# Optimization experiments

Measured on AMD Instinct MI355X. Metric: run time of the kernel, lower is better.

## Reference

```python
import jax, jax.numpy as jnp
import numpy as np

H = 51  # n_hidden
B = 8192  # batch
T = 2048  # seq_len
FUTURE = 64


def setup_inputs() -> dict:
    key = jax.random.key(0)
    ks = jax.random.split(key, 12)
    s = 1.0 / np.sqrt(H)
    u = lambda k, shape: jax.random.uniform(k, shape, jnp.float32, -s, s)
    return {
        "x": jax.random.normal(ks[0], (B, T), jnp.float32),
        "W_ih1": u(ks[1], (4 * H, 1)),
        "W_hh1": u(ks[2], (4 * H, H)),
        "b_ih1": u(ks[3], (4 * H,)),
        "b_hh1": u(ks[4], (4 * H,)),
        "W_ih2": u(ks[5], (4 * H, H)),
        "W_hh2": u(ks[6], (4 * H, H)),
        "b_ih2": u(ks[7], (4 * H,)),
        "b_hh2": u(ks[8], (4 * H,)),
        "W_out": u(ks[9], (1, H)),
        "b_out": u(ks[10], (1,)),
        "future": FUTURE,
    }


def _lstm_cell(x, h, c, Wih, Whh, bih, bhh):
    # PyTorch LSTMCell: gates ordered i, f, g, o
    g = x @ Wih.T + h @ Whh.T + (bih + bhh)  # [B, 4H]
    i, f, gg, o = jnp.split(g, 4, axis=-1)
    i = jax.nn.sigmoid(i)
    f = jax.nn.sigmoid(f)
    gg = jnp.tanh(gg)
    o = jax.nn.sigmoid(o)
    c2 = f * c + i * gg
    h2 = o * jnp.tanh(c2)
    return h2, c2


def reference(x, W_ih1, W_hh1, b_ih1, b_hh1, W_ih2, W_hh2, b_ih2, b_hh2,
              W_out, b_out, future):
    Bn = x.shape[0]
    h1 = jnp.zeros((Bn, H), x.dtype)
    c1 = jnp.zeros((Bn, H), x.dtype)

    def emit(h1, c1):
        # Quirk of the original code: layer-2 state is layer-1's CURRENT (h1, c1),
        # and layer-2's own state is never carried forward.
        h2, _ = _lstm_cell(h1, h1, c1, W_ih2, W_hh2, b_ih2, b_hh2)
        return h2 @ W_out.T + b_out  # [B, 1]

    def step(carry, xt):
        h1, c1 = carry
        h1, c1 = _lstm_cell(xt, h1, c1, W_ih1, W_hh1, b_ih1, b_hh1)
        out = emit(h1, c1)
        return (h1, c1), out

    xs = jnp.swapaxes(x, 0, 1)[:, :, None]  # [T, B, 1]
    (h1, c1), outs = jax.lax.scan(step, (h1, c1), xs)
    outs = outs[..., 0].T  # [B, T]

    def fstep(carry, _):
        h1, c1, out = carry
        h1, c1 = _lstm_cell(out, h1, c1, W_ih1, W_hh1, b_ih1, b_hh1)
        out = emit(h1, c1)
        return (h1, c1, out), out

    last = outs[:, -1:]
    _, fouts = jax.lax.scan(fstep, (h1, c1, last), None, length=future)
    fouts = fouts[..., 0].T if future > 0 else jnp.zeros((Bn, 0), x.dtype)
    return jnp.concatenate([outs, fouts], axis=1)  # [B, T + future]
```

## Files before the change

### kernel.cpp

```cpp
#include <hip/hip_runtime.h>

#define HH   51
#define H4   204
#define TSEQ 2048
#define FUT  64
#define TT   (TSEQ + FUT)
#define RPB  16
#define NTH  1024
#define HSTR 72

typedef _Float16 h8 __attribute__((ext_vector_type(8)));
typedef float    f4 __attribute__((ext_vector_type(4)));

#define LOG2E 1.44269504f
#define MFMA(a, b, c) __builtin_amdgcn_mfma_f32_16x16x32_f16(a, b, c, 0, 0, 0)

__device__ __forceinline__ void act_cell(const f4 g, float cin, float* cout, float* hout) {
    const float ei = __builtin_amdgcn_exp2f(g[0]);
    const float ef = __builtin_amdgcn_exp2f(g[1]);
    const float eg = __builtin_amdgcn_exp2f(g[2]);
    const float eo = __builtin_amdgcn_exp2f(g[3]);
    const float A = 1.0f + ei, B = 1.0f + ef, G = 1.0f + eg, C = 1.0f + eo;
    const float rAB = __builtin_amdgcn_rcpf(A * B);
    const float ig = rAB * B;
    const float fg = rAB * A;
    const float rGC = __builtin_amdgcn_rcpf(G * C);
    const float og = rGC * G;
    const float tg = __builtin_fmaf(2.0f, rGC * C, -1.0f);
    const float c2 = __builtin_fmaf(fg, cin, ig * tg);
    const float ec = __builtin_amdgcn_exp2f(-2.0f * LOG2E * c2);
    const float th = __builtin_fmaf(2.0f, __builtin_amdgcn_rcpf(1.0f + ec), -1.0f);
    *cout = c2;
    *hout = og * th;
}

#define MERGED_BODY(P, EMIT_IDX, DO_EMIT, XI)                                      \
    do {                                                                           \
        if (is_comp) {                                                             \
            const h8 b0 = *(const h8*)&hbuf[P][nl][quad * 8];                      \
            const h8 b1 = *(const h8*)&hbuf[P][nl][32 + quad * 8];                 \
            f4 G1 = {0.f, 0.f, 0.f, 0.f}, G2 = {0.f, 0.f, 0.f, 0.f};               \
            G2 = MFMA(W2[0], b0, G2); G2 = MFMA(W2[1], b1, G2);                    \
            G1 = MFMA(W1[0], b0, G1); G1 = MFMA(W1[1], b1, G1);                    \
            float c2v, h2v;                                                        \
            act_cell(G2, c1, &c2v, &h2v);         \
            part[(P) ^ 1][cw][quad][nl] = h2v * wo;                                \
            float hv;                                                              \
            act_cell(G1, c1, &c1, &hv);                     \
            if (kh < HH) hbuf[(P) ^ 1][nl][1 + kh] = (_Float16)hv;                 \
        } else if (w == we) {                                                      \
            if ((DO_EMIT) && lane < RPB) {                                         \
                float s0 = bo, s1 = 0.f, s2 = 0.f, s3 = 0.f;                       \
                _Pragma("unroll")                                                  \
                for (int j = 0; j < 13; ++j) {                                     \
                    s0 += part[P][j][0][lane];                                     \
                    s1 += part[P][j][1][lane];                                     \
                    s2 += part[P][j][2][lane];                                     \
                    s3 += part[P][j][3][lane];                                     \
                }                                                                  \
                out[(size_t)(rb + lane) * TT + (EMIT_IDX)] = (s0 + s1) + (s2 + s3);\
            }                                                                      \
        } else if (w == wp && lane < RPB) {                                        \
            if ((XI) + 1 < TSEQ) hbuf[(P) ^ 1][lane][0] = (_Float16)xnext;         \
            if ((XI) + 2 < TSEQ) xnext = x[(size_t)(rb + lane) * TSEQ + (XI) + 2]; \
        }                                                                          \
        __syncthreads();                                                           \
    } while (0)

__global__ __launch_bounds__(NTH, 8)
void lstm_kernel(const float* __restrict__ x,
                 const float* __restrict__ Wih1, const float* __restrict__ Whh1,
                 const float* __restrict__ bih1, const float* __restrict__ bhh1,
                 const float* __restrict__ Wih2, const float* __restrict__ Whh2,
                 const float* __restrict__ bih2, const float* __restrict__ bhh2,
                 const float* __restrict__ Wout, const float* __restrict__ bout,
                 float* __restrict__ out)
{
    __shared__ _Float16 hbuf[2][RPB][HSTR];
    __shared__ float part[2][13][4][17];
    __shared__ float wouts[64];

    const int tid  = threadIdx.x;
    const int lane = tid & 63;
    const int w    = tid >> 6;
    const int quad = lane >> 4;
    const int nl   = lane & 15;
    const int rb   = blockIdx.x * RPB;

    const int  rot     = (blockIdx.x >> 8) & 1;
    const int  cw      = w - (rot ? 3 : 0);
    const bool is_comp = (cw >= 0) && (cw < 13);
    const int  we      = rot ? 0 : 13;
    const int  wp      = rot ? 1 : 14;

    if (tid < 64) wouts[tid] = (tid < HH) ? Wout[tid] : 0.0f;
    for (int i = tid; i < 2 * RPB * HSTR; i += NTH) (&hbuf[0][0][0])[i] = (_Float16)0.0f;
    __syncthreads();
    if (tid < RPB) {
        hbuf[0][tid][0]  = (_Float16)x[(size_t)(rb + tid) * TSEQ];
        hbuf[0][tid][52] = (_Float16)1.0f;  hbuf[0][tid][53] = (_Float16)1.0f;
        hbuf[1][tid][52] = (_Float16)1.0f;  hbuf[1][tid][53] = (_Float16)1.0f;
    }
    const float bo = bout[0];

    h8 W1[2], W2[2];
    if (is_comp) {
        const int jp = 16 * cw + nl;
        const int kk = jp >> 2, q = jp & 3;
        const bool valid = (jp < H4);
        const int jrow = q * HH + kk;
        const float sc = (q == 2) ? (-2.0f * LOG2E) : (-LOG2E);
        float b1 = 0.0f, b2 = 0.0f;
        if (valid) { b1 = sc * (bih1[jrow] + bhh1[jrow]); b2 = sc * (bih2[jrow] + bhh2[jrow]); }
        const _Float16 b1h = (_Float16)b1, b2h = (_Float16)b2;
        const _Float16 b1l = (_Float16)(b1 - (float)b1h), b2l = (_Float16)(b2 - (float)b2h);
        #pragma unroll
        for (int s = 0; s < 2; ++s) {
            h8 w1v, w2v;
            #pragma unroll
            for (int j = 0; j < 8; ++j) {
                const int k = s * 32 + quad * 8 + j;
                _Float16 a1 = (_Float16)0.0f, a2 = (_Float16)0.0f;
                if (valid) {
                    if (k == 0) {
                        a1 = (_Float16)(sc * Wih1[jrow]);
                    } else if (k <= HH) {
                        const int o = jrow * HH + (k - 1);
                        a1 = (_Float16)(sc * Whh1[o]);
                        a2 = (_Float16)(sc * (Wih2[o] + Whh2[o]));
                    } else if (k == 52) { a1 = b1h; a2 = b2h; }
                    else if (k == 53)   { a1 = b1l; a2 = b2l; }
                }
                w1v[j] = a1;
                w2v[j] = a2;
            }
            W1[s] = w1v;
            W2[s] = w2v;
        }
    }

    float xnext = 0.0f;
    if (w == wp && lane < RPB) xnext = x[(size_t)(rb + lane) * TSEQ + 1];

    const int kh = 4 * cw + quad;
    float c1 = 0.0f;
    __syncthreads();
    const float wo = is_comp ? wouts[kh] : 0.0f;

    if (is_comp) {
        const h8 b0 = *(const h8*)&hbuf[0][nl][quad * 8];
        const h8 b1 = *(const h8*)&hbuf[0][nl][32 + quad * 8];
        f4 G1 = {0.f, 0.f, 0.f, 0.f};
        G1 = MFMA(W1[0], b0, G1); G1 = MFMA(W1[1], b1, G1);
        float hv;
        act_cell(G1, c1, &c1, &hv);
        if (kh < HH) hbuf[1][nl][1 + kh] = (_Float16)hv;
    } else if (w == wp && lane < RPB) {
        hbuf[1][lane][0] = (_Float16)xnext;
        xnext = x[(size_t)(rb + lane) * TSEQ + 2];
    }
    __syncthreads();

    MERGED_BODY(1, 0, false, 1);

    for (int i = 2; i < TSEQ; i += 2) {
        MERGED_BODY(0, i - 2, true, i);
        MERGED_BODY(1, i - 1, true, i + 1);
    }

    for (int t = TSEQ - 1; t < TT; ++t) {
        const int pb = (t + 1) & 1;
        if (is_comp) {
            const h8 b0 = *(const h8*)&hbuf[pb][nl][quad * 8];
            const h8 b1 = *(const h8*)&hbuf[pb][nl][32 + quad * 8];
            f4 G2 = {0.f, 0.f, 0.f, 0.f};
            G2 = MFMA(W2[0], b0, G2); G2 = MFMA(W2[1], b1, G2);
            float c2v, h2v;
            act_cell(G2, c1, &c2v, &h2v);
            part[t & 1][cw][quad][nl] = h2v * wo;
        } else if (w == we && t == TSEQ - 1 && lane < RPB) {
            float s0 = bo, s1 = 0.f, s2 = 0.f, s3 = 0.f;
            #pragma unroll
            for (int j = 0; j < 13; ++j) {
                s0 += part[0][j][0][lane];
                s1 += part[0][j][1][lane];
                s2 += part[0][j][2][lane];
                s3 += part[0][j][3][lane];
            }
            out[(size_t)(rb + lane) * TT + (TSEQ - 2)] = (s0 + s1) + (s2 + s3);
        }
        __syncthreads();
        if (w == we && lane < RPB) {
            float s0 = bo, s1 = 0.f, s2 = 0.f, s3 = 0.f;
            #pragma unroll
            for (int j = 0; j < 13; ++j) {
                s0 += part[t & 1][j][0][lane];
                s1 += part[t & 1][j][1][lane];
                s2 += part[t & 1][j][2][lane];
                s3 += part[t & 1][j][3][lane];
            }
            const float s = (s0 + s1) + (s2 + s3);
            out[(size_t)(rb + lane) * TT + t] = s;
            if (t + 1 < TT) hbuf[pb][lane][0] = (_Float16)s;
        }
        __syncthreads();
        if (t + 1 < TT) {
            if (is_comp) {
                const h8 b0 = *(const h8*)&hbuf[pb][nl][quad * 8];
                const h8 b1 = *(const h8*)&hbuf[pb][nl][32 + quad * 8];
                f4 G1 = {0.f, 0.f, 0.f, 0.f};
                G1 = MFMA(W1[0], b0, G1); G1 = MFMA(W1[1], b1, G1);
                float hv;
                act_cell(G1, c1, &c1, &hv);
                if (kh < HH) hbuf[pb ^ 1][nl][1 + kh] = (_Float16)hv;
            }
            __syncthreads();
        }
    }
}

extern "C" void kernel_launch(void* const* d_in, const int* in_sizes, int n_in,
                              void* d_out, int out_size, void* d_ws, size_t ws_size,
                              hipStream_t stream) {
    (void)in_sizes; (void)n_in; (void)d_ws; (void)ws_size; (void)out_size;
    const float* x    = (const float*)d_in[0];
    const float* Wih1 = (const float*)d_in[1];
    const float* Whh1 = (const float*)d_in[2];
    const float* bih1 = (const float*)d_in[3];
    const float* bhh1 = (const float*)d_in[4];
    const float* Wih2 = (const float*)d_in[5];
    const float* Whh2 = (const float*)d_in[6];
    const float* bih2 = (const float*)d_in[7];
    const float* bhh2 = (const float*)d_in[8];
    const float* Wout = (const float*)d_in[9];
    const float* bout = (const float*)d_in[10];
    float* outp = (float*)d_out;

    dim3 grid(8192 / RPB);
    dim3 block(NTH);
    hipLaunchKernelGGL(lstm_kernel, grid, block, 0, stream,
                       x, Wih1, Whh1, bih1, bhh1, Wih2, Whh2, bih2, bhh2,
                       Wout, bout, outp);
}
```

Baseline: 2.502 ms.

## Defer layer-2 emit activation by one step and merge aux warps

```diff
diff --git a/kernel.cpp b/kernel.cpp
--- a/kernel.cpp
+++ b/kernel.cpp
@@ -6,7 +6,7 @@
 #define FUT  64
 #define TT   (TSEQ + FUT)
 #define RPB  16
-#define NTH  1024
+#define NTH  896
 #define HSTR 72
 
 typedef _Float16 h8 __attribute__((ext_vector_type(8)));
@@ -34,35 +34,54 @@
     *hout = og * th;
 }
 
-#define MERGED_BODY(P, EMIT_IDX, DO_EMIT, XI)                                      \
+__device__ __forceinline__ void act_emit(const f4 g, float cin, float* hout) {
+    const float ei = __builtin_amdgcn_exp2f(g[0]);
+    const float ef = __builtin_amdgcn_exp2f(g[1]);
+    const float eg = __builtin_amdgcn_exp2f(g[2]);
+    const float eo = __builtin_amdgcn_exp2f(g[3]);
+    const float A = 1.0f + ei, B = 1.0f + ef, G = 1.0f + eg, C = 1.0f + eo;
+    const float P1 = A * B, P2 = G * C;
+    const float r = __builtin_amdgcn_rcpf(P1 * P2);
+    const float rP2 = r * P2, rP1 = r * P1;
+    const float ig = rP2 * B;
+    const float fg = rP2 * A;
+    const float og = rP1 * G;
+    const float tg = __builtin_fmaf(2.0f, rP1 * C, -1.0f);
+    const float c2 = __builtin_fmaf(fg, cin, ig * tg);
+    const float ec = __builtin_amdgcn_exp2f(-2.0f * LOG2E * c2);
+    const float th = __builtin_fmaf(2.0f, __builtin_amdgcn_rcpf(1.0f + ec), -1.0f);
+    *hout = og * th;
+}
+
+#define MBODY(P, i)                                                                \
     do {                                                                           \
         if (is_comp) {                                                             \
             const h8 b0 = *(const h8*)&hbuf[P][nl][quad * 8];                      \
             const h8 b1 = *(const h8*)&hbuf[P][nl][32 + quad * 8];                 \
-            f4 G1 = {0.f, 0.f, 0.f, 0.f}, G2 = {0.f, 0.f, 0.f, 0.f};               \
+            float h2v;                                                             \
+            act_emit(G2d, c1d, &h2v);                                              \
+            part[P][cw][quad][nl] = h2v * wo;                                      \
+            f4 G2 = {0.f, 0.f, 0.f, 0.f}, G1 = {0.f, 0.f, 0.f, 0.f};               \
             G2 = MFMA(W2[0], b0, G2); G2 = MFMA(W2[1], b1, G2);                    \
             G1 = MFMA(W1[0], b0, G1); G1 = MFMA(W1[1], b1, G1);                    \
-            float c2v, h2v;                                                        \
-            act_cell(G2, c1, &c2v, &h2v);         \
-            part[(P) ^ 1][cw][quad][nl] = h2v * wo;                                \
+            G2d = G2; c1d = c1;                                                    \
             float hv;                                                              \
-            act_cell(G1, c1, &c1, &hv);                     \
+            act_cell(G1, c1, &c1, &hv);                                            \
             if (kh < HH) hbuf[(P) ^ 1][nl][1 + kh] = (_Float16)hv;                 \
-        } else if (w == we) {                                                      \
-            if ((DO_EMIT) && lane < RPB) {                                         \
+        } else if (w == wa && lane < RPB) {                                        \
+            if ((i) >= 3) {                                                        \
                 float s0 = bo, s1 = 0.f, s2 = 0.f, s3 = 0.f;                       \
                 _Pragma("unroll")                                                  \
                 for (int j = 0; j < 13; ++j) {                                     \
-                    s0 += part[P][j][0][lane];                                     \
-                    s1 += part[P][j][1][lane];                                     \
-                    s2 += part[P][j][2][lane];                                     \
-                    s3 += part[P][j][3][lane];                                     \
+                    s0 += part[(P) ^ 1][j][0][lane];                               \
+                    s1 += part[(P) ^ 1][j][1][lane];                               \
+                    s2 += part[(P) ^ 1][j][2][lane];                               \
+                    s3 += part[(P) ^ 1][j][3][lane];                               \
                 }                                                                  \
-                out[(size_t)(rb + lane) * TT + (EMIT_IDX)] = (s0 + s1) + (s2 + s3);\
+                out[(size_t)(rb + lane) * TT + (i) - 3] = (s0 + s1) + (s2 + s3);   \
             }                                                                      \
-        } else if (w == wp && lane < RPB) {                                        \
-            if ((XI) + 1 < TSEQ) hbuf[(P) ^ 1][lane][0] = (_Float16)xnext;         \
-            if ((XI) + 2 < TSEQ) xnext = x[(size_t)(rb + lane) * TSEQ + (XI) + 2]; \
+            if ((i) + 1 < TSEQ) hbuf[(P) ^ 1][lane][0] = (_Float16)xnext;          \
+            if ((i) + 2 < TSEQ) xnext = x[(size_t)(rb + lane) * TSEQ + (i) + 2];   \
         }                                                                          \
         __syncthreads();                                                           \
     } while (0)
@@ -88,10 +107,9 @@
     const int rb   = blockIdx.x * RPB;
 
     const int  rot     = (blockIdx.x >> 8) & 1;
-    const int  cw      = w - (rot ? 3 : 0);
+    const int  cw      = w - rot;
     const bool is_comp = (cw >= 0) && (cw < 13);
-    const int  we      = rot ? 0 : 13;
-    const int  wp      = rot ? 1 : 14;
+    const int  wa      = rot ? 0 : 13;
 
     if (tid < 64) wouts[tid] = (tid < HH) ? Wout[tid] : 0.0f;
     for (int i = tid; i < 2 * RPB * HSTR; i += NTH) (&hbuf[0][0][0])[i] = (_Float16)0.0f;
@@ -140,10 +158,12 @@
     }
 
     float xnext = 0.0f;
-    if (w == wp && lane < RPB) xnext = x[(size_t)(rb + lane) * TSEQ + 1];
+    if (w == wa && lane < RPB) xnext = x[(size_t)(rb + lane) * TSEQ + 1];
 
     const int kh = 4 * cw + quad;
     float c1 = 0.0f;
+    f4 G2d = {0.f, 0.f, 0.f, 0.f};
+    float c1d = 0.0f;
     __syncthreads();
     const float wo = is_comp ? wouts[kh] : 0.0f;
 
@@ -155,18 +175,49 @@
         float hv;
         act_cell(G1, c1, &c1, &hv);
         if (kh < HH) hbuf[1][nl][1 + kh] = (_Float16)hv;
-    } else if (w == wp && lane < RPB) {
+    } else if (w == wa && lane < RPB) {
         hbuf[1][lane][0] = (_Float16)xnext;
         xnext = x[(size_t)(rb + lane) * TSEQ + 2];
     }
     __syncthreads();
 
-    MERGED_BODY(1, 0, false, 1);
+    if (is_comp) {
+        const h8 b0 = *(const h8*)&hbuf[1][nl][quad * 8];
+        const h8 b1 = *(const h8*)&hbuf[1][nl][32 + quad * 8];
+        f4 G2 = {0.f, 0.f, 0.f, 0.f}, G1 = {0.f, 0.f, 0.f, 0.f};
+        G2 = MFMA(W2[0], b0, G2); G2 = MFMA(W2[1], b1, G2);
+        G1 = MFMA(W1[0], b0, G1); G1 = MFMA(W1[1], b1, G1);
+        G2d = G2; c1d = c1;
+        float hv;
+        act_cell(G1, c1, &c1, &hv);
+        if (kh < HH) hbuf[0][nl][1 + kh] = (_Float16)hv;
+    } else if (w == wa && lane < RPB) {
+        hbuf[0][lane][0] = (_Float16)xnext;
+        xnext = x[(size_t)(rb + lane) * TSEQ + 3];
+    }
+    __syncthreads();
 
     for (int i = 2; i < TSEQ; i += 2) {
-        MERGED_BODY(0, i - 2, true, i);
-        MERGED_BODY(1, i - 1, true, i + 1);
-    }
+        MBODY(0, i);
+        MBODY(1, i + 1);
+    }
+
+    if (is_comp) {
+        float h2v;
+        act_emit(G2d, c1d, &h2v);
+        part[0][cw][quad][nl] = h2v * wo;
+    } else if (w == wa && lane < RPB) {
+        float s0 = bo, s1 = 0.f, s2 = 0.f, s3 = 0.f;
+        #pragma unroll
+        for (int j = 0; j < 13; ++j) {
+            s0 += part[1][j][0][lane];
+            s1 += part[1][j][1][lane];
+            s2 += part[1][j][2][lane];
+            s3 += part[1][j][3][lane];
+        }
+        out[(size_t)(rb + lane) * TT + (TSEQ - 3)] = (s0 + s1) + (s2 + s3);
+    }
+    __syncthreads();
 
     for (int t = TSEQ - 1; t < TT; ++t) {
         const int pb = (t + 1) & 1;
@@ -175,10 +226,10 @@
             const h8 b1 = *(const h8*)&hbuf[pb][nl][32 + quad * 8];
             f4 G2 = {0.f, 0.f, 0.f, 0.f};
             G2 = MFMA(W2[0], b0, G2); G2 = MFMA(W2[1], b1, G2);
-            float c2v, h2v;
-            act_cell(G2, c1, &c2v, &h2v);
+            float h2v;
+            act_emit(G2, c1, &h2v);
             part[t & 1][cw][quad][nl] = h2v * wo;
-        } else if (w == we && t == TSEQ - 1 && lane < RPB) {
+        } else if (w == wa && t == TSEQ - 1 && lane < RPB) {
             float s0 = bo, s1 = 0.f, s2 = 0.f, s3 = 0.f;
             #pragma unroll
             for (int j = 0; j < 13; ++j) {
@@ -190,7 +241,7 @@
             out[(size_t)(rb + lane) * TT + (TSEQ - 2)] = (s0 + s1) + (s2 + s3);
         }
         __syncthreads();
-        if (w == we && lane < RPB) {
+        if (w == wa && lane < RPB) {
             float s0 = bo, s1 = 0.f, s2 = 0.f, s3 = 0.f;
             #pragma unroll
             for (int j = 0; j < 13; ++j) {
```

Result: slower. 2.994 ms (+19.6%).
